# Kernel optimization log

Measured on AMD Instinct MI355X. Metric: run time of the kernel, lower is better.

Reference implementation:

```python
import jax, jax.numpy as jnp
from jax import lax
import numpy as np

B, T, N, F_IN, H, E, K = 8, 32, 500, 64, 128, 8000, 3
LN_EPS = 1e-5


def setup_inputs() -> dict:
    key = jax.random.key(0)
    ks = jax.random.split(key, 10)
    x = jax.random.normal(ks[0], (B, T, N, F_IN), dtype=jnp.float32)
    edge_index = jax.random.randint(ks[1], (2, E), 0, N, dtype=jnp.int64)
    edge_weight = jax.random.uniform(ks[2], (E,), dtype=jnp.float32)
    # GCNConv: linear (in->out) + bias
    W_gcn = jax.random.normal(ks[3], (F_IN, H), dtype=jnp.float32) / np.sqrt(F_IN)
    b_gcn = jnp.zeros((H,), dtype=jnp.float32)
    # Conv1d(H, H, K): weight (O, I, K)
    W_temp = jax.random.normal(ks[4], (H, H, K), dtype=jnp.float32) / np.sqrt(H * K)
    b_temp = jnp.zeros((H,), dtype=jnp.float32)
    # LayerNorm(H)
    ln_w = jnp.ones((H,), dtype=jnp.float32)
    ln_b = jnp.zeros((H,), dtype=jnp.float32)
    # residual Linear (in->out)
    W_res = jax.random.normal(ks[5], (F_IN, H), dtype=jnp.float32) / np.sqrt(F_IN)
    b_res = jnp.zeros((H,), dtype=jnp.float32)
    return {"x": x, "edge_index": edge_index, "edge_weight": edge_weight,
            "W_gcn": W_gcn, "b_gcn": b_gcn, "W_temp": W_temp, "b_temp": b_temp,
            "ln_w": ln_w, "ln_b": ln_b, "W_res": W_res, "b_res": b_res}


def reference(x, edge_index, edge_weight, W_gcn, b_gcn, W_temp, b_temp, ln_w, ln_b, W_res, b_res):
    Bv, Tv, Nv, Fv = x.shape
    Hv = W_gcn.shape[1]
    res = x @ W_res + b_res  # (B,T,N,H)

    # ---- spatial GCNConv on B*T replicated graphs (vectorized, no index offsetting) ----
    xf = x.reshape(Bv * Tv, Nv, Fv) @ W_gcn  # (BT,N,H)
    src, dst = edge_index[0], edge_index[1]
    loops = jnp.arange(Nv, dtype=edge_index.dtype)
    src2 = jnp.concatenate([src, loops])
    dst2 = jnp.concatenate([dst, loops])
    ew2 = jnp.concatenate([edge_weight, jnp.ones((Nv,), dtype=edge_weight.dtype)])
    deg = jax.ops.segment_sum(ew2, dst2, num_segments=Nv)
    dinv = jnp.where(deg > 0, deg ** -0.5, 0.0)
    norm = dinv[src2] * ew2 * dinv[dst2]  # (E+N,)
    msgs = xf[:, src2, :] * norm[None, :, None]  # (BT, E+N, H)
    agg = jax.vmap(lambda m: jax.ops.segment_sum(m, dst2, num_segments=Nv))(msgs)
    h = jax.nn.gelu(agg + b_gcn, approximate=False)  # (BT,N,H)

    # ---- temporal Conv1d over T ----
    h = h.reshape(Bv, Tv, Nv, Hv).transpose(0, 2, 3, 1).reshape(Bv * Nv, Hv, Tv)
    pad = K // 2
    h = lax.conv_general_dilated(h, W_temp, window_strides=(1,), padding=[(pad, pad)],
                                 dimension_numbers=("NCH", "OIH", "NCH"))
    h = jax.nn.gelu(h + b_temp[None, :, None], approximate=False)
    h = h.reshape(Bv, Nv, Hv, Tv).transpose(0, 3, 1, 2)  # (B,T,N,H)

    # ---- fused residual + LayerNorm over last dim ----
    y = h + res
    mu = jnp.mean(y, axis=-1, keepdims=True)
    var = jnp.mean((y - mu) ** 2, axis=-1, keepdims=True)
    return (y - mu) * lax.rsqrt(var + LN_EPS) * ln_w + ln_b
```

## Files before the change

kernel.cpp:

```cpp
#include <hip/hip_runtime.h>
#include <hip/hip_bf16.h>
#include <math.h>

#define Bv 8
#define Tv 32
#define Nv 500
#define Fin 64
#define Hv 128
#define Ev 8000
#define Kv 3
#define BT (Bv*Tv)
#define ROWS (BT*Nv)
#define TP (Tv+2)
#define KK (Kv*Hv)
#define LDSROW 144

typedef __attribute__((ext_vector_type(8))) short s8v;
typedef __attribute__((ext_vector_type(4))) float f4v;

__device__ __forceinline__ float gelu_exact(float v){
    return 0.5f*v*(1.0f + erff(v*0.70710678118654752440f));
}
__device__ __forceinline__ short f2bs(float f){
    union { __hip_bfloat16 h; short s; } u;
    u.h = __float2bfloat16(f);
    return u.s;
}
__device__ __forceinline__ float b2f(short s){
    union { unsigned int i; float f; } u;
    u.i = ((unsigned int)(unsigned short)s) << 16;
    return u.f;
}

__global__ __launch_bounds__(1024) void k_prep(const int* __restrict__ ei,
        const float* __restrict__ ew, float* __restrict__ dinv,
        int* __restrict__ offs, int* __restrict__ csrc, float* __restrict__ cw){
    __shared__ float sdeg[Nv];
    __shared__ int   scnt[Nv];
    __shared__ float sdv[Nv];
    __shared__ int   scur[Nv];
    __shared__ int   sa[512], sb[512];
    int tid = threadIdx.x;
    if (tid < Nv){ sdeg[tid] = 1.0f; scnt[tid] = 0; }
    __syncthreads();
    for (int e = tid; e < Ev; e += 1024){
        int d = ei[Ev + e];
        atomicAdd(&sdeg[d], ew[e]);
        atomicAdd(&scnt[d], 1);
    }
    __syncthreads();
    int c = 0;
    if (tid < Nv){
        float d = sdeg[tid];
        float v = (d > 0.f) ? rsqrtf(d) : 0.f;
        sdv[tid] = v; dinv[tid] = v;
    }
    if (tid < 512){ c = (tid < Nv) ? scnt[tid] : 0; sa[tid] = c; }
    __syncthreads();
    int* s = sa; int* t = sb;
    for (int off = 1; off < 512; off <<= 1){
        int v = 0;
        if (tid < 512){ v = s[tid]; if (tid >= off) v += s[tid - off]; }
        if (tid < 512) t[tid] = v;
        __syncthreads();
        int* tmp = s; s = t; t = tmp;
    }
    if (tid < Nv){ int excl = s[tid] - c; offs[tid] = excl; scur[tid] = excl; }
    if (tid == 0) offs[Nv] = Ev;
    __syncthreads();
    for (int e = tid; e < Ev; e += 1024){
        int sn = ei[e], d = ei[Ev + e];
        int pos = atomicAdd(&scur[d], 1);
        csrc[pos] = sn;
        cw[pos] = sdv[sn]*ew[e]*sdv[d];
    }
}

__global__ __launch_bounds__(256) void k_xpose(const float* __restrict__ x,
        short* __restrict__ X2b, const float* __restrict__ W,
        const float* __restrict__ Wg, const float* __restrict__ Wr,
        short* __restrict__ W2, short* __restrict__ Wgt, short* __restrict__ Wrt){
    int bid = blockIdx.x;
    if (bid < ROWS/16){
        int gid = bid*256 + threadIdx.x;
        int row = gid >> 4, c4 = gid & 15;
        int bt = row / Nv;
        int n  = row - bt*Nv;
        float4 v = ((const float4*)x)[gid];
        short4 sv;
        sv.x = f2bs(v.x); sv.y = f2bs(v.y); sv.z = f2bs(v.z); sv.w = f2bs(v.w);
        *(short4*)(X2b + (size_t)n*(BT*64) + bt*64 + c4*4) = sv;
    } else {
        int idx = (bid - ROWS/16)*256 + threadIdx.x;
        if (idx < Hv*Hv*Kv){
            int o = idx/(Hv*Kv);
            int rem = idx - o*(Hv*Kv);
            int i = rem/Kv, k = rem - i*Kv;
            W2[o*KK + k*Hv + i] = f2bs(W[idx]);
        } else if (idx < Hv*Hv*Kv + Hv*64){
            int j = idx - Hv*Hv*Kv;
            int o = j >> 6, k = j & 63;
            Wgt[j] = f2bs(Wg[k*Hv + o]);
        } else if (idx < Hv*Hv*Kv + 2*Hv*64){
            int j = idx - Hv*Hv*Kv - Hv*64;
            int o = j >> 6, k = j & 63;
            Wrt[j] = f2bs(Wr[k*Hv + o]);
        }
    }
}

__global__ __launch_bounds__(256) void k_spmm(const short* __restrict__ X2b,
        const float* __restrict__ dinv, const int* __restrict__ offs,
        const int* __restrict__ csrc, const float* __restrict__ cw,
        short* __restrict__ AGG2){
    int bid = blockIdx.x;
    int ct = bid / Nv;
    int n  = bid - ct*Nv;
    int col = ct*2048 + threadIdx.x*8;
    float dv = dinv[n];
    float sw = dv*dv;
    float acc[8];
    s8v v = *(const s8v*)(X2b + (size_t)n*(BT*64) + col);
    #pragma unroll
    for (int q = 0; q < 8; ++q) acc[q] = sw * b2f(v[q]);
    int e0 = offs[n], e1 = offs[n+1];
    for (int e = e0; e < e1; ++e){
        int s = csrc[e]; float w = cw[e];
        s8v u = *(const s8v*)(X2b + (size_t)s*(BT*64) + col);
        #pragma unroll
        for (int q = 0; q < 8; ++q) acc[q] = fmaf(w, b2f(u[q]), acc[q]);
    }
    s8v r;
    #pragma unroll
    for (int q = 0; q < 8; ++q) r[q] = f2bs(acc[q]);
    *(s8v*)(AGG2 + (size_t)n*(BT*64) + col) = r;
}

__global__ __launch_bounds__(256, 2) void k_mega(
        const short* __restrict__ AGG2, const short* __restrict__ X2b,
        const short* __restrict__ W2, const short* __restrict__ Wgt,
        const short* __restrict__ Wrt,
        const float* __restrict__ bg, const float* __restrict__ btm,
        const float* __restrict__ br, const float* __restrict__ lw,
        const float* __restrict__ lb, float* __restrict__ out){
    __shared__ short hs[4*TP*LDSROW];
    __shared__ float red[Tv][4][2];
    int tid  = threadIdx.x;
    int w    = tid >> 6;
    int lane = tid & 63;
    int quad = lane >> 4;
    int laneo = lane & 15;
    int bid = blockIdx.x;
    int b  = bid / 125;
    int n0 = (bid - b*125) * 4;
    int o_base = w*32;

    float bgv[2], bbv[2], brv[2], lwv[2], lbv[2];
    #pragma unroll
    for (int nt = 0; nt < 2; ++nt){
        int o = o_base + nt*16 + laneo;
        bgv[nt] = bg[o]; bbv[nt] = btm[o]; brv[nt] = br[o];
        lwv[nt] = lw[o]; lbv[nt] = lb[o];
    }

    s8v bwg[2][2];
    #pragma unroll
    for (int nt = 0; nt < 2; ++nt){
        const short* wp = Wgt + (o_base + nt*16 + laneo)*64 + quad*8;
        bwg[nt][0] = *(const s8v*)wp;
        bwg[nt][1] = *(const s8v*)(wp + 32);
    }

    if (tid < 128){
        int node = tid >> 5, rem = tid & 31;
        int tp = (rem >> 4)*(TP-1), c8 = rem & 15;
        s8v z = {0,0,0,0,0,0,0,0};
        *(s8v*)&hs[node*(TP*LDSROW) + tp*LDSROW + c8*8] = z;
    }

    for (int g = 0; g < 4; ++g){
        int n = n0 + g;
        const short* ap = AGG2 + ((size_t)n*BT + b*Tv)*64;
        #pragma unroll
        for (int m = 0; m < 2; ++m){
            const short* arp = ap + (m*16 + laneo)*64 + quad*8;
            s8v a0 = *(const s8v*)arp;
            s8v a1 = *(const s8v*)(arp + 32);
            f4v h0 = {0.f,0.f,0.f,0.f}, h1 = {0.f,0.f,0.f,0.f};
            h0 = __builtin_amdgcn_mfma_f32_16x16x32_bf16(a0, bwg[0][0], h0, 0,0,0);
            h0 = __builtin_amdgcn_mfma_f32_16x16x32_bf16(a1, bwg[0][1], h0, 0,0,0);
            h1 = __builtin_amdgcn_mfma_f32_16x16x32_bf16(a0, bwg[1][0], h1, 0,0,0);
            h1 = __builtin_amdgcn_mfma_f32_16x16x32_bf16(a1, bwg[1][1], h1, 0,0,0);
            #pragma unroll
            for (int r = 0; r < 4; ++r){
                int tp = m*16 + quad*4 + r + 1;
                short* hrow = &hs[g*(TP*LDSROW) + tp*LDSROW];
                hrow[o_base + laneo]      = f2bs(gelu_exact(h0[r] + bgv[0]));
                hrow[o_base + 16 + laneo] = f2bs(gelu_exact(h1[r] + bgv[1]));
            }
        }
    }

    s8v breg[2][12], bwr[2][2];
    #pragma unroll
    for (int nt = 0; nt < 2; ++nt){
        int o = o_base + nt*16 + laneo;
        const short* wp = W2 + o*KK + quad*8;
        #pragma unroll
        for (int s = 0; s < 12; ++s)
            breg[nt][s] = *(const s8v*)(wp + s*32);
        const short* wr = Wrt + o*64 + quad*8;
        bwr[nt][0] = *(const s8v*)wr;
        bwr[nt][1] = *(const s8v*)(wr + 32);
    }
    __syncthreads();

    for (int g = 0; g < 4; ++g){
        int n = n0 + g;
        f4v acc[2][2];
        #pragma unroll
        for (int m = 0; m < 2; ++m)
            #pragma unroll
            for (int nt = 0; nt < 2; ++nt)
                acc[m][nt] = (f4v){0.f,0.f,0.f,0.f};
        #pragma unroll
        for (int m = 0; m < 2; ++m){
            #pragma unroll
            for (int s = 0; s < 12; ++s){
                int k  = s >> 2;
                int i0 = (s & 3) * 32;
                int tp = m*16 + laneo + k;
                s8v a = *(const s8v*)&hs[g*(TP*LDSROW) + tp*LDSROW + i0 + quad*8];
                acc[m][0] = __builtin_amdgcn_mfma_f32_16x16x32_bf16(a, breg[0][s], acc[m][0], 0,0,0);
                acc[m][1] = __builtin_amdgcn_mfma_f32_16x16x32_bf16(a, breg[1][s], acc[m][1], 0,0,0);
            }
        }
        f4v racc[2][2];
        #pragma unroll
        for (int m = 0; m < 2; ++m)
            #pragma unroll
            for (int nt = 0; nt < 2; ++nt)
                racc[m][nt] = (f4v){0.f,0.f,0.f,0.f};
        const short* xp = X2b + ((size_t)n*BT + b*Tv)*64;
        #pragma unroll
        for (int m = 0; m < 2; ++m){
            const short* xrp = xp + (m*16 + laneo)*64 + quad*8;
            s8v a0 = *(const s8v*)xrp;
            s8v a1 = *(const s8v*)(xrp + 32);
            racc[m][0] = __builtin_amdgcn_mfma_f32_16x16x32_bf16(a0, bwr[0][0], racc[m][0], 0,0,0);
            racc[m][0] = __builtin_amdgcn_mfma_f32_16x16x32_bf16(a1, bwr[0][1], racc[m][0], 0,0,0);
            racc[m][1] = __builtin_amdgcn_mfma_f32_16x16x32_bf16(a0, bwr[1][0], racc[m][1], 0,0,0);
            racc[m][1] = __builtin_amdgcn_mfma_f32_16x16x32_bf16(a1, bwr[1][1], racc[m][1], 0,0,0);
        }
        size_t obase = ((size_t)b*Tv*Nv + n)*Hv;
        float yv[2][2][4];
        float srow[2][4], ssrow[2][4];
        #pragma unroll
        for (int m = 0; m < 2; ++m)
            #pragma unroll
            for (int r = 0; r < 4; ++r){ srow[m][r] = 0.f; ssrow[m][r] = 0.f; }
        #pragma unroll
        for (int m = 0; m < 2; ++m){
            #pragma unroll
            for (int nt = 0; nt < 2; ++nt){
                #pragma unroll
                for (int r = 0; r < 4; ++r){
                    float gv = gelu_exact(acc[m][nt][r] + bbv[nt]);
                    float y = gv + racc[m][nt][r] + brv[nt];
                    yv[m][nt][r] = y;
                    srow[m][r] += y; ssrow[m][r] += y*y;
                }
            }
        }
        #pragma unroll
        for (int m = 0; m < 2; ++m)
            #pragma unroll
            for (int r = 0; r < 4; ++r){
                #pragma unroll
                for (int msk = 8; msk >= 1; msk >>= 1){
                    srow[m][r]  += __shfl_xor(srow[m][r],  msk, 64);
                    ssrow[m][r] += __shfl_xor(ssrow[m][r], msk, 64);
                }
            }
        if (laneo == 0){
            #pragma unroll
            for (int m = 0; m < 2; ++m)
                #pragma unroll
                for (int r = 0; r < 4; ++r){
                    int t = m*16 + quad*4 + r;
                    red[t][w][0] = srow[m][r];
                    red[t][w][1] = ssrow[m][r];
                }
        }
        __syncthreads();
        #pragma unroll
        for (int m = 0; m < 2; ++m){
            #pragma unroll
            for (int r = 0; r < 4; ++r){
                int t = m*16 + quad*4 + r;
                float s  = red[t][0][0] + red[t][1][0] + red[t][2][0] + red[t][3][0];
                float ss = red[t][0][1] + red[t][1][1] + red[t][2][1] + red[t][3][1];
                float mu = s * (1.f/128.f);
                float var = fmaxf(ss * (1.f/128.f) - mu*mu, 0.f);
                float rstd = rsqrtf(var + 1e-5f);
                #pragma unroll
                for (int nt = 0; nt < 2; ++nt){
                    int o = o_base + nt*16 + laneo;
                    out[obase + (size_t)t*Nv*Hv + o] =
                        (yv[m][nt][r] - mu)*rstd*lwv[nt] + lbv[nt];
                }
            }
        }
        __syncthreads();
    }
}

extern "C" void kernel_launch(void* const* d_in, const int* in_sizes, int n_in,
                              void* d_out, int out_size, void* d_ws, size_t ws_size,
                              hipStream_t stream){
    const float* x   = (const float*)d_in[0];
    const int*   ei  = (const int*)d_in[1];
    const float* ew  = (const float*)d_in[2];
    const float* Wg  = (const float*)d_in[3];
    const float* bg  = (const float*)d_in[4];
    const float* Wtm = (const float*)d_in[5];
    const float* btm = (const float*)d_in[6];
    const float* lw  = (const float*)d_in[7];
    const float* lb  = (const float*)d_in[8];
    const float* Wr  = (const float*)d_in[9];
    const float* br  = (const float*)d_in[10];
    float* out = (float*)d_out;

    char* ws = (char*)d_ws;
    float* dinv = (float*)(ws + 0);
    int*   offs = (int*)  (ws + 4096);
    int*   csrc = (int*)  (ws + 8192);
    float* cwn  = (float*)(ws + 40960);
    short* W2   = (short*)(ws + 73728);
    short* Wgt  = (short*)(ws + 172032);
    short* Wrt  = (short*)(ws + 188416);
    short* X2b  = (short*)(ws + 204800);
    short* AGG2 = (short*)(ws + 16588800);

    k_prep <<<1, 1024, 0, stream>>>(ei, ew, dinv, offs, csrc, cwn);
    k_xpose<<<ROWS/16 + 256, 256, 0, stream>>>(x, X2b, Wtm, Wg, Wr, W2, Wgt, Wrt);
    k_spmm <<<8*Nv, 256, 0, stream>>>(X2b, dinv, offs, csrc, cwn, AGG2);
    k_mega <<<(Bv*Nv)/4, 256, 0, stream>>>(AGG2, X2b, W2, Wgt, Wrt,
                                           bg, btm, br, lw, lb, out);
}
```

Baseline: 219.3 us.

## Merge graph prep into transpose kernel, approximate GELU, remap spmm blocks, raise occupancy

The graph CSR preparation kernel is merged into the input/weight transpose kernel as block 0, removing one launch and letting the single-block prep run alongside the transpose blocks. Exact erf in GELU is replaced by the Abramowitz-Stegun polynomial with fast rcp/exp, cutting transcendental cost at the price of roughly 1e-7 absolute erf error. The spmm block index now places the eight column tiles of one node in consecutive blocks for better cache locality. The fused mega kernel's launch bounds request 4 blocks per CU instead of 2, which may push it into register spills.

Measured after the change: 265.5 us. 1.21x slower.

```diff
diff --git a/kernel.cpp b/kernel.cpp
--- a/kernel.cpp
+++ b/kernel.cpp
@@ -19,7 +19,15 @@
 typedef __attribute__((ext_vector_type(4))) float f4v;
 
 __device__ __forceinline__ float gelu_exact(float v){
-    return 0.5f*v*(1.0f + erff(v*0.70710678118654752440f));
+    float t  = v*0.70710678118654752440f;
+    float ax = fabsf(t);
+    float k  = __builtin_amdgcn_rcpf(fmaf(0.3275911f, ax, 1.0f));
+    float p  = k*fmaf(k, fmaf(k, fmaf(k, fmaf(k, 1.061405429f, -1.453152027f),
+                                      1.421413741f), -0.284496736f), 0.254829592f);
+    float e  = __expf(-ax*ax);
+    float er = fmaf(-p, e, 1.0f);
+    er = copysignf(er, t);
+    return 0.5f*v*(1.0f + er);
 }
 __device__ __forceinline__ short f2bs(float f){
     union { __hip_bfloat16 h; short s; } u;
@@ -32,57 +40,56 @@
     return u.f;
 }
 
-__global__ __launch_bounds__(1024) void k_prep(const int* __restrict__ ei,
-        const float* __restrict__ ew, float* __restrict__ dinv,
-        int* __restrict__ offs, int* __restrict__ csrc, float* __restrict__ cw){
+__global__ __launch_bounds__(1024) void k_xprep(const float* __restrict__ x,
+        short* __restrict__ X2b, const float* __restrict__ W,
+        const float* __restrict__ Wg, const float* __restrict__ Wr,
+        short* __restrict__ W2, short* __restrict__ Wgt, short* __restrict__ Wrt,
+        const int* __restrict__ ei, const float* __restrict__ ew,
+        float* __restrict__ dinv, int* __restrict__ offs,
+        int* __restrict__ csrc, float* __restrict__ cw){
     __shared__ float sdeg[Nv];
     __shared__ int   scnt[Nv];
     __shared__ float sdv[Nv];
     __shared__ int   scur[Nv];
     __shared__ int   sa[512], sb[512];
+    int bid = blockIdx.x;
     int tid = threadIdx.x;
-    if (tid < Nv){ sdeg[tid] = 1.0f; scnt[tid] = 0; }
-    __syncthreads();
-    for (int e = tid; e < Ev; e += 1024){
-        int d = ei[Ev + e];
-        atomicAdd(&sdeg[d], ew[e]);
-        atomicAdd(&scnt[d], 1);
-    }
-    __syncthreads();
-    int c = 0;
-    if (tid < Nv){
-        float d = sdeg[tid];
-        float v = (d > 0.f) ? rsqrtf(d) : 0.f;
-        sdv[tid] = v; dinv[tid] = v;
-    }
-    if (tid < 512){ c = (tid < Nv) ? scnt[tid] : 0; sa[tid] = c; }
-    __syncthreads();
-    int* s = sa; int* t = sb;
-    for (int off = 1; off < 512; off <<= 1){
-        int v = 0;
-        if (tid < 512){ v = s[tid]; if (tid >= off) v += s[tid - off]; }
-        if (tid < 512) t[tid] = v;
-        __syncthreads();
-        int* tmp = s; s = t; t = tmp;
-    }
-    if (tid < Nv){ int excl = s[tid] - c; offs[tid] = excl; scur[tid] = excl; }
-    if (tid == 0) offs[Nv] = Ev;
-    __syncthreads();
-    for (int e = tid; e < Ev; e += 1024){
-        int sn = ei[e], d = ei[Ev + e];
-        int pos = atomicAdd(&scur[d], 1);
-        csrc[pos] = sn;
-        cw[pos] = sdv[sn]*ew[e]*sdv[d];
-    }
-}
-
-__global__ __launch_bounds__(256) void k_xpose(const float* __restrict__ x,
-        short* __restrict__ X2b, const float* __restrict__ W,
-        const float* __restrict__ Wg, const float* __restrict__ Wr,
-        short* __restrict__ W2, short* __restrict__ Wgt, short* __restrict__ Wrt){
-    int bid = blockIdx.x;
-    if (bid < ROWS/16){
-        int gid = bid*256 + threadIdx.x;
+    if (bid == 0){
+        if (tid < Nv){ sdeg[tid] = 1.0f; scnt[tid] = 0; }
+        __syncthreads();
+        for (int e = tid; e < Ev; e += 1024){
+            int d = ei[Ev + e];
+            atomicAdd(&sdeg[d], ew[e]);
+            atomicAdd(&scnt[d], 1);
+        }
+        __syncthreads();
+        int c = 0;
+        if (tid < Nv){
+            float d = sdeg[tid];
+            float v = (d > 0.f) ? rsqrtf(d) : 0.f;
+            sdv[tid] = v; dinv[tid] = v;
+        }
+        if (tid < 512){ c = (tid < Nv) ? scnt[tid] : 0; sa[tid] = c; }
+        __syncthreads();
+        int* s = sa; int* t = sb;
+        for (int off = 1; off < 512; off <<= 1){
+            int v = 0;
+            if (tid < 512){ v = s[tid]; if (tid >= off) v += s[tid - off]; }
+            if (tid < 512) t[tid] = v;
+            __syncthreads();
+            int* tmp = s; s = t; t = tmp;
+        }
+        if (tid < Nv){ int excl = s[tid] - c; offs[tid] = excl; scur[tid] = excl; }
+        if (tid == 0) offs[Nv] = Ev;
+        __syncthreads();
+        for (int e = tid; e < Ev; e += 1024){
+            int sn = ei[e], d = ei[Ev + e];
+            int pos = atomicAdd(&scur[d], 1);
+            csrc[pos] = sn;
+            cw[pos] = sdv[sn]*ew[e]*sdv[d];
+        }
+    } else if (bid <= ROWS/64){
+        int gid = (bid-1)*1024 + tid;
         int row = gid >> 4, c4 = gid & 15;
         int bt = row / Nv;
         int n  = row - bt*Nv;
@@ -91,7 +98,7 @@
         sv.x = f2bs(v.x); sv.y = f2bs(v.y); sv.z = f2bs(v.z); sv.w = f2bs(v.w);
         *(short4*)(X2b + (size_t)n*(BT*64) + bt*64 + c4*4) = sv;
     } else {
-        int idx = (bid - ROWS/16)*256 + threadIdx.x;
+        int idx = (bid - 1 - ROWS/64)*1024 + tid;
         if (idx < Hv*Hv*Kv){
             int o = idx/(Hv*Kv);
             int rem = idx - o*(Hv*Kv);
@@ -114,8 +121,8 @@
         const int* __restrict__ csrc, const float* __restrict__ cw,
         short* __restrict__ AGG2){
     int bid = blockIdx.x;
-    int ct = bid / Nv;
-    int n  = bid - ct*Nv;
+    int ct = bid & 7;
+    int n  = bid >> 3;
     int col = ct*2048 + threadIdx.x*8;
     float dv = dinv[n];
     float sw = dv*dv;
@@ -136,7 +143,7 @@
     *(s8v*)(AGG2 + (size_t)n*(BT*64) + col) = r;
 }
 
-__global__ __launch_bounds__(256, 2) void k_mega(
+__global__ __launch_bounds__(256, 4) void k_mega(
         const short* __restrict__ AGG2, const short* __restrict__ X2b,
         const short* __restrict__ W2, const short* __restrict__ Wgt,
         const short* __restrict__ Wrt,
@@ -342,8 +349,9 @@
     short* X2b  = (short*)(ws + 204800);
     short* AGG2 = (short*)(ws + 16588800);
 
-    k_prep <<<1, 1024, 0, stream>>>(ei, ew, dinv, offs, csrc, cwn);
-    k_xpose<<<ROWS/16 + 256, 256, 0, stream>>>(x, X2b, Wtm, Wg, Wr, W2, Wgt, Wrt);
+    k_xprep<<<1 + ROWS/64 + 64, 1024, 0, stream>>>(x, X2b, Wtm, Wg, Wr,
+                                                   W2, Wgt, Wrt,
+                                                   ei, ew, dinv, offs, csrc, cwn);
     k_spmm <<<8*Nv, 256, 0, stream>>>(X2b, dinv, offs, csrc, cwn, AGG2);
     k_mega <<<(Bv*Nv)/4, 256, 0, stream>>>(AGG2, X2b, W2, Wgt, Wrt,
                                            bg, btm, br, lw, lb, out);
```
